# Optimization experiments

Measured on AMD Instinct MI355X. Metric: run time of the kernel, lower is better.

The kernel has to match this reference:

```python
import jax, jax.numpy as jnp
import numpy as np

D_MODEL = 1024
NUM_HEADS = 16
D_K = D_MODEL // NUM_HEADS


def setup_inputs() -> dict:
    key = jax.random.key(0)
    ks = jax.random.split(key, 16)
    B, S, D = 4, 2048, D_MODEL
    scale = 1.0 / np.sqrt(D)
    inp = {
        'Xs': jax.random.normal(ks[0], (B, S, D), jnp.float32),
        'Xt': jax.random.normal(ks[1], (B, S, D), jnp.float32),
    }
    names = ['qs', 'qt', 'ks', 'kt', 'vs', 'vt']
    for i, n in enumerate(names):
        inp['W_' + n] = jax.random.normal(ks[2 + 2 * i], (D, D), jnp.float32) * scale
        inp['b_' + n] = jax.random.normal(ks[3 + 2 * i], (D,), jnp.float32) * 0.01
    inp['attn_bias'] = jnp.zeros((1, 1, 1, 1), jnp.float32)
    return inp


def _split_heads(x):
    B, S, _ = x.shape
    return x.reshape(B, S, NUM_HEADS, D_K).transpose(0, 2, 1, 3)  # (B,H,S,dk)


def reference(Xs, Xt, W_qs, b_qs, W_qt, b_qt, W_ks, b_ks, W_kt, b_kt,
              W_vs, b_vs, W_vt, b_vt, attn_bias):
    # Dual-linear fused projections: Linear(x) = x @ W.T + b (torch convention)
    Q = Xs @ W_qs.T + b_qs + Xt @ W_qt.T + b_qt
    K = Xs @ W_ks.T + b_ks + Xt @ W_kt.T + b_kt
    V = Xs @ W_vs.T + b_vs + Xt @ W_vt.T + b_vt
    Q, K, V = _split_heads(Q), _split_heads(K), _split_heads(V)
    scores = jnp.einsum('bhqd,bhkd->bhqk', Q, K) / jnp.sqrt(jnp.float32(D_K))
    scores = scores + attn_bias  # scalar learned bias, broadcast
    probs = jax.nn.softmax(scores, axis=-1)
    out = jnp.einsum('bhqk,bhkd->bhqd', probs, V)  # (B,H,S,dk)
    B, H, S, dk = out.shape
    return out.transpose(0, 2, 1, 3).reshape(B, S, H * dk)
```

## Files before the change

kernel.cpp:

```cpp
#include <hip/hip_runtime.h>
#include <hip/hip_bf16.h>

typedef __bf16 bf16;
typedef __attribute__((ext_vector_type(8))) __bf16 bf16x8;
typedef __attribute__((ext_vector_type(4))) __bf16 bf16x4;
typedef __attribute__((ext_vector_type(4))) float f32x4;

#define D_MODEL 1024
#define NHEAD 16
#define DK 64
#define BB 4
#define SS 2048
#define MM 8192
#define KK 2048
#define NN 3072

#define LDP 72
#define QSCALE 0.18033688011112042f

__device__ __forceinline__ void glds16(const bf16* g, bf16* s) {
    __builtin_amdgcn_global_load_lds(
        (const __attribute__((address_space(1))) void*)g,
        (__attribute__((address_space(3))) void*)s, 16, 0, 0);
}

__global__ void cast_pack(const float* __restrict__ src, bf16* __restrict__ dst,
                          int row_off, int col_off, int nchunks) {
    int i = blockIdx.x * 256 + threadIdx.x;
    if (i >= nchunks) return;
    int m = i >> 7;
    int cl = i & 127;
    const float4* s4 = (const float4*)&src[((size_t)m << 10) + cl * 8];
    float4 v0 = s4[0], v1 = s4[1];
    bf16x8 o;
    o[0]=(bf16)v0.x; o[1]=(bf16)v0.y; o[2]=(bf16)v0.z; o[3]=(bf16)v0.w;
    o[4]=(bf16)v1.x; o[5]=(bf16)v1.y; o[6]=(bf16)v1.z; o[7]=(bf16)v1.w;
    int r = row_off + m;
    int k = col_off + cl * 8;
    int mi = r & 127, mt = r >> 7;
    int c = (k >> 3) & 7, kt = k >> 6;
    int slot = mi * 8 + (c ^ (mi & 7));
    *(bf16x8*)&dst[(((((size_t)mt * 32 + kt) << 10) + slot) << 3)] = o;
}

__global__ void bias_cat_k(const float* __restrict__ bqs, const float* __restrict__ bqt,
                           const float* __restrict__ bks, const float* __restrict__ bkt,
                           const float* __restrict__ bvs, const float* __restrict__ bvt,
                           float* __restrict__ out) {
    int n = blockIdx.x * 256 + threadIdx.x;
    int g = n >> 10, c = n & 1023;
    const float* a = (g == 0) ? bqs : ((g == 1) ? bks : bvs);
    const float* b = (g == 0) ? bqt : ((g == 1) ? bkt : bvt);
    out[n] = a[c] + b[c];
}

__global__ __launch_bounds__(256) void gemm_qkv(
    const bf16* __restrict__ Xp, const bf16* __restrict__ Wp,
    const float* __restrict__ biasc,
    bf16* __restrict__ Qb, bf16* __restrict__ Kb, bf16* __restrict__ Vt) {
    __shared__ __align__(16) bf16 sA[128 * 64];
    __shared__ __align__(16) bf16 sB[128 * 64];

    const int m0 = blockIdx.x * 128, n0 = blockIdx.y * 128;
    const int t = threadIdx.x, lane = t & 63, w = t >> 6;
    const int quad = lane >> 4, l16 = lane & 15, swz = l16 & 7;
    const int wm = (w >> 1) * 64, wn = (w & 1) * 64;

    f32x4 acc[4][4] = {};

    for (int ktI = 0; ktI < 32; ktI++) {
        const bf16* Ab = Xp + (((size_t)blockIdx.x * 32 + ktI) << 13);
        const bf16* Bb = Wp + (((size_t)blockIdx.y * 32 + ktI) << 13);
#pragma unroll
        for (int j = 0; j < 4; j++) {
            int u = (w * 4 + j) * 64 + lane;
            glds16(Ab + (size_t)u * 8, &sA[(w * 4 + j) * 512]);
            glds16(Bb + (size_t)u * 8, &sB[(w * 4 + j) * 512]);
        }
        __syncthreads();
#pragma unroll
        for (int kb = 0; kb < 2; kb++) {
            bf16x8 af[4], bfr[4];
#pragma unroll
            for (int mi = 0; mi < 4; mi++)
                af[mi] = *(const bf16x8*)&sA[(wm + mi * 16 + l16) * 64 + (((kb * 4 + quad) ^ swz) * 8)];
#pragma unroll
            for (int ni = 0; ni < 4; ni++)
                bfr[ni] = *(const bf16x8*)&sB[(wn + ni * 16 + l16) * 64 + (((kb * 4 + quad) ^ swz) * 8)];
#pragma unroll
            for (int mi = 0; mi < 4; mi++)
#pragma unroll
                for (int ni = 0; ni < 4; ni++)
                    acc[mi][ni] = __builtin_amdgcn_mfma_f32_16x16x32_bf16(
                        af[mi], bfr[ni], acc[mi][ni], 0, 0, 0);
        }
        __syncthreads();
    }

    const int g = n0 >> 10;
    for (int mi = 0; mi < 4; mi++) {
        int mbase = m0 + wm + mi * 16 + quad * 4;
        for (int ni = 0; ni < 4; ni++) {
            int n = n0 + wn + ni * 16 + l16;
            float bias = biasc[n];
            int c = n & 1023, h = c >> 6, d = c & 63;
            for (int r = 0; r < 4; r++) {
                int m = mbase + r;
                int b = m >> 11, s = m & 2047;
                size_t bh = (size_t)(b * NHEAD + h);
                float v = acc[mi][ni][r] + bias;
                if (g == 0)
                    Qb[(bh * SS + s) * DK + d] = (bf16)(v * QSCALE);
                else if (g == 1)
                    Kb[(bh * SS + s) * DK + d] = (bf16)v;
                else
                    Vt[(bh * DK + d) * SS + s] = (bf16)v;
            }
        }
    }
}

__global__ __launch_bounds__(256) void attn(
    const bf16* __restrict__ Qb, const bf16* __restrict__ Kb,
    const bf16* __restrict__ Vt, float* __restrict__ out) {
    __shared__ __align__(16) bf16 sK[64 * 64];
    __shared__ __align__(16) bf16 sV[64 * 64];
    __shared__ __align__(16) bf16 sP[4][32 * LDP];

    const int q0 = blockIdx.x * 128;
    const int bh = blockIdx.y;
    const int t = threadIdx.x;
    const int lane = t & 63, w = t >> 6;
    const int quad = lane >> 4, l16 = lane & 15, swz = l16 & 7;
    const int b = bh >> 4, h = bh & 15;

    const bf16* Qp = Qb + ((size_t)bh * SS + q0 + w * 32) * DK;
    bf16x8 qf[2][2];
#pragma unroll
    for (int f = 0; f < 2; f++)
#pragma unroll
        for (int kb = 0; kb < 2; kb++)
            qf[f][kb] = *(const bf16x8*)&Qp[(f * 16 + l16) * DK + kb * 32 + quad * 8];

    f32x4 o[2][4] = {};
    float lsum[2] = {0.f, 0.f};

    const bf16* Kp = Kb + (size_t)bh * SS * DK;
    const bf16* Vp = Vt + (size_t)bh * DK * SS;

    for (int kt = 0; kt < SS; kt += 64) {
#pragma unroll
        for (int j = 0; j < 2; j++) {
            int u = (w * 2 + j) * 64 + lane;
            int row = u >> 3;
            int cc = (u & 7) ^ (row & 7);
            glds16(Kp + (size_t)(kt + row) * DK + cc * 8, &sK[(w * 2 + j) * 512]);
            glds16(Vp + (size_t)row * SS + kt + cc * 8, &sV[(w * 2 + j) * 512]);
        }
        __syncthreads();

        f32x4 st[2][4] = {};
#pragma unroll
        for (int kb = 0; kb < 2; kb++)
#pragma unroll
            for (int ki = 0; ki < 4; ki++) {
                bf16x8 kf = *(const bf16x8*)&sK[(ki * 16 + l16) * 64 + (((kb * 4 + quad) ^ swz) * 8)];
                st[0][ki] = __builtin_amdgcn_mfma_f32_16x16x32_bf16(kf, qf[0][kb], st[0][ki], 0, 0, 0);
                st[1][ki] = __builtin_amdgcn_mfma_f32_16x16x32_bf16(kf, qf[1][kb], st[1][ki], 0, 0, 0);
            }

#pragma unroll
        for (int f = 0; f < 2; f++) {
            float ls = 0.f;
#pragma unroll
            for (int ki = 0; ki < 4; ki++) {
                float p0 = __builtin_amdgcn_exp2f(st[f][ki][0]);
                float p1 = __builtin_amdgcn_exp2f(st[f][ki][1]);
                float p2 = __builtin_amdgcn_exp2f(st[f][ki][2]);
                float p3 = __builtin_amdgcn_exp2f(st[f][ki][3]);
                ls += (p0 + p1) + (p2 + p3);
                bf16x4 pk;
                pk[0] = (bf16)p0; pk[1] = (bf16)p1; pk[2] = (bf16)p2; pk[3] = (bf16)p3;
                *(bf16x4*)&sP[w][(f * 16 + l16) * LDP + ki * 16 + quad * 4] = pk;
            }
            lsum[f] += ls;
        }

#pragma unroll
        for (int kb = 0; kb < 2; kb++) {
            bf16x8 af0 = *(const bf16x8*)&sP[w][(l16) * LDP + kb * 32 + quad * 8];
            bf16x8 af1 = *(const bf16x8*)&sP[w][(16 + l16) * LDP + kb * 32 + quad * 8];
#pragma unroll
            for (int ni = 0; ni < 4; ni++) {
                bf16x8 vf = *(const bf16x8*)&sV[(ni * 16 + l16) * 64 + (((kb * 4 + quad) ^ swz) * 8)];
                o[0][ni] = __builtin_amdgcn_mfma_f32_16x16x32_bf16(af0, vf, o[0][ni], 0, 0, 0);
                o[1][ni] = __builtin_amdgcn_mfma_f32_16x16x32_bf16(af1, vf, o[1][ni], 0, 0, 0);
            }
        }
        __syncthreads();
    }

#pragma unroll
    for (int f = 0; f < 2; f++) {
        lsum[f] += __shfl_xor(lsum[f], 16);
        lsum[f] += __shfl_xor(lsum[f], 32);
    }

    float* op = out + ((size_t)(b * SS + q0 + w * 32)) * D_MODEL + h * DK;
#pragma unroll
    for (int f = 0; f < 2; f++)
#pragma unroll
        for (int r = 0; r < 4; r++) {
            float linv = 1.0f / __shfl(lsum[f], quad * 4 + r);
#pragma unroll
            for (int ni = 0; ni < 4; ni++)
                op[(f * 16 + quad * 4 + r) * D_MODEL + ni * 16 + l16] = o[f][ni][r] * linv;
        }
}

extern "C" void kernel_launch(void* const* d_in, const int* in_sizes, int n_in,
                              void* d_out, int out_size, void* d_ws, size_t ws_size,
                              hipStream_t stream) {
    const float* Xs   = (const float*)d_in[0];
    const float* Xt   = (const float*)d_in[1];
    const float* Wqs  = (const float*)d_in[2];
    const float* bqs  = (const float*)d_in[3];
    const float* Wqt  = (const float*)d_in[4];
    const float* bqt  = (const float*)d_in[5];
    const float* Wks  = (const float*)d_in[6];
    const float* bks  = (const float*)d_in[7];
    const float* Wkt  = (const float*)d_in[8];
    const float* bkt  = (const float*)d_in[9];
    const float* Wvs  = (const float*)d_in[10];
    const float* bvs  = (const float*)d_in[11];
    const float* Wvt  = (const float*)d_in[12];
    const float* bvt  = (const float*)d_in[13];
    float* out = (float*)d_out;

    char* ws = (char*)d_ws;
    bf16*  Xp    = (bf16*)(ws);
    bf16*  Wp    = (bf16*)(ws + 33554432);
    float* biasc = (float*)(ws + 46137344);
    bf16*  Qb    = (bf16*)(ws + 46149632);
    bf16*  Kb    = (bf16*)(ws + 62926848);
    bf16*  Vt    = (bf16*)(ws + 79704064);

    {
        int nchunks = MM * 128;
        int blocks = nchunks / 256;
        cast_pack<<<blocks, 256, 0, stream>>>(Xs, Xp, 0, 0, nchunks);
        cast_pack<<<blocks, 256, 0, stream>>>(Xt, Xp, 0, 1024, nchunks);
    }
    {
        int nchunks = 1024 * 128;
        int blocks = nchunks / 256;
        const float* Wsrc_s[3] = {Wqs, Wks, Wvs};
        const float* Wsrc_t[3] = {Wqt, Wkt, Wvt};
        for (int gi = 0; gi < 3; gi++) {
            cast_pack<<<blocks, 256, 0, stream>>>(Wsrc_s[gi], Wp, gi * 1024, 0, nchunks);
            cast_pack<<<blocks, 256, 0, stream>>>(Wsrc_t[gi], Wp, gi * 1024, 1024, nchunks);
        }
    }
    bias_cat_k<<<12, 256, 0, stream>>>(bqs, bqt, bks, bkt, bvs, bvt, biasc);

    gemm_qkv<<<dim3(MM / 128, NN / 128), 256, 0, stream>>>(Xp, Wp, biasc, Qb, Kb, Vt);

    attn<<<dim3(SS / 128, BB * NHEAD), 256, 0, stream>>>(Qb, Kb, Vt, out);
}
```

Baseline: 381.1 us.

## Double attention query tile per block and merge cast/bias kernels

The attention kernel now gives each block 256 queries, 64 rows per wave, instead of 128. K and V fragments are loaded from shared memory once into registers and reused across four query row-groups, which halves the total K/V global loads and LDS reads per query. The eight cast_pack launches plus the bias kernel are merged into two launches to cut launch overhead. In exchange the attention grid shrinks to 512 blocks and register and LDS use per block rise, which may lower occupancy and latency hiding.

Result: slower. 400.9 us (+5.2%).

```diff
diff --git a/kernel.cpp b/kernel.cpp
--- a/kernel.cpp
+++ b/kernel.cpp
@@ -24,12 +24,11 @@
         (__attribute__((address_space(3))) void*)s, 16, 0, 0);
 }
 
-__global__ void cast_pack(const float* __restrict__ src, bf16* __restrict__ dst,
-                          int row_off, int col_off, int nchunks) {
-    int i = blockIdx.x * 256 + threadIdx.x;
-    if (i >= nchunks) return;
-    int m = i >> 7;
-    int cl = i & 127;
+__device__ __forceinline__ void pack_chunk(const float* __restrict__ src,
+                                           bf16* __restrict__ dst,
+                                           int row_off, int col_off, int idx) {
+    int m = idx >> 7;
+    int cl = idx & 127;
     const float4* s4 = (const float4*)&src[((size_t)m << 10) + cl * 8];
     float4 v0 = s4[0], v1 = s4[1];
     bf16x8 o;
@@ -43,15 +42,36 @@
     *(bf16x8*)&dst[(((((size_t)mt * 32 + kt) << 10) + slot) << 3)] = o;
 }
 
-__global__ void bias_cat_k(const float* __restrict__ bqs, const float* __restrict__ bqt,
-                           const float* __restrict__ bks, const float* __restrict__ bkt,
-                           const float* __restrict__ bvs, const float* __restrict__ bvt,
-                           float* __restrict__ out) {
-    int n = blockIdx.x * 256 + threadIdx.x;
-    int g = n >> 10, c = n & 1023;
-    const float* a = (g == 0) ? bqs : ((g == 1) ? bks : bvs);
-    const float* b = (g == 0) ? bqt : ((g == 1) ? bkt : bvt);
-    out[n] = a[c] + b[c];
+__global__ void pack_x(const float* __restrict__ Xs, const float* __restrict__ Xt,
+                       bf16* __restrict__ dst) {
+    int i = blockIdx.x * 256 + threadIdx.x;
+    int sel = i >> 20;
+    int idx = i & 1048575;
+    pack_chunk(sel ? Xt : Xs, dst, 0, sel ? 1024 : 0, idx);
+}
+
+__global__ void pack_w(const float* __restrict__ Wqs, const float* __restrict__ Wqt,
+                       const float* __restrict__ Wks, const float* __restrict__ Wkt,
+                       const float* __restrict__ Wvs, const float* __restrict__ Wvt,
+                       const float* __restrict__ bqs, const float* __restrict__ bqt,
+                       const float* __restrict__ bks, const float* __restrict__ bkt,
+                       const float* __restrict__ bvs, const float* __restrict__ bvt,
+                       bf16* __restrict__ dst, float* __restrict__ biasc) {
+    if (blockIdx.x == 3072) {
+        for (int n = threadIdx.x; n < NN; n += 256) {
+            int g = n >> 10, c = n & 1023;
+            const float* a = (g == 0) ? bqs : ((g == 1) ? bks : bvs);
+            const float* b = (g == 0) ? bqt : ((g == 1) ? bkt : bvt);
+            biasc[n] = a[c] + b[c];
+        }
+        return;
+    }
+    int i = blockIdx.x * 256 + threadIdx.x;
+    int gi = i >> 17;
+    int idx = i & 131071;
+    const float* src = (gi == 0) ? Wqs : (gi == 1) ? Wqt : (gi == 2) ? Wks
+                     : (gi == 3) ? Wkt : (gi == 4) ? Wvs : Wvt;
+    pack_chunk(src, dst, (gi >> 1) * 1024, (gi & 1) * 1024, idx);
 }
 
 __global__ __launch_bounds__(256) void gemm_qkv(
@@ -125,25 +145,25 @@
     const bf16* __restrict__ Vt, float* __restrict__ out) {
     __shared__ __align__(16) bf16 sK[64 * 64];
     __shared__ __align__(16) bf16 sV[64 * 64];
-    __shared__ __align__(16) bf16 sP[4][32 * LDP];
-
-    const int q0 = blockIdx.x * 128;
+    __shared__ __align__(16) bf16 sP[4][64 * LDP];
+
+    const int q0 = blockIdx.x * 256;
     const int bh = blockIdx.y;
     const int t = threadIdx.x;
     const int lane = t & 63, w = t >> 6;
     const int quad = lane >> 4, l16 = lane & 15, swz = l16 & 7;
     const int b = bh >> 4, h = bh & 15;
 
-    const bf16* Qp = Qb + ((size_t)bh * SS + q0 + w * 32) * DK;
-    bf16x8 qf[2][2];
-#pragma unroll
-    for (int f = 0; f < 2; f++)
+    const bf16* Qp = Qb + ((size_t)bh * SS + q0 + w * 64) * DK;
+    bf16x8 qf[4][2];
+#pragma unroll
+    for (int f = 0; f < 4; f++)
 #pragma unroll
         for (int kb = 0; kb < 2; kb++)
             qf[f][kb] = *(const bf16x8*)&Qp[(f * 16 + l16) * DK + kb * 32 + quad * 8];
 
-    f32x4 o[2][4] = {};
-    float lsum[2] = {0.f, 0.f};
+    f32x4 o[4][4] = {};
+    float lsum[4] = {0.f, 0.f, 0.f, 0.f};
 
     const bf16* Kp = Kb + (size_t)bh * SS * DK;
     const bf16* Vp = Vt + (size_t)bh * DK * SS;
@@ -159,25 +179,30 @@
         }
         __syncthreads();
 
-        f32x4 st[2][4] = {};
+        bf16x8 kf[2][4];
 #pragma unroll
         for (int kb = 0; kb < 2; kb++)
 #pragma unroll
+            for (int ki = 0; ki < 4; ki++)
+                kf[kb][ki] = *(const bf16x8*)&sK[(ki * 16 + l16) * 64 + (((kb * 4 + quad) ^ swz) * 8)];
+
+#pragma unroll
+        for (int f = 0; f < 4; f++) {
+            f32x4 st[4] = {};
+#pragma unroll
+            for (int kb = 0; kb < 2; kb++)
+#pragma unroll
+                for (int ki = 0; ki < 4; ki++)
+                    st[ki] = __builtin_amdgcn_mfma_f32_16x16x32_bf16(
+                        kf[kb][ki], qf[f][kb], st[ki], 0, 0, 0);
+
+            float ls = 0.f;
+#pragma unroll
             for (int ki = 0; ki < 4; ki++) {
-                bf16x8 kf = *(const bf16x8*)&sK[(ki * 16 + l16) * 64 + (((kb * 4 + quad) ^ swz) * 8)];
-                st[0][ki] = __builtin_amdgcn_mfma_f32_16x16x32_bf16(kf, qf[0][kb], st[0][ki], 0, 0, 0);
-                st[1][ki] = __builtin_amdgcn_mfma_f32_16x16x32_bf16(kf, qf[1][kb], st[1][ki], 0, 0, 0);
-            }
-
-#pragma unroll
-        for (int f = 0; f < 2; f++) {
-            float ls = 0.f;
-#pragma unroll
-            for (int ki = 0; ki < 4; ki++) {
-                float p0 = __builtin_amdgcn_exp2f(st[f][ki][0]);
-                float p1 = __builtin_amdgcn_exp2f(st[f][ki][1]);
-                float p2 = __builtin_amdgcn_exp2f(st[f][ki][2]);
-                float p3 = __builtin_amdgcn_exp2f(st[f][ki][3]);
+                float p0 = __builtin_amdgcn_exp2f(st[ki][0]);
+                float p1 = __builtin_amdgcn_exp2f(st[ki][1]);
+                float p2 = __builtin_amdgcn_exp2f(st[ki][2]);
+                float p3 = __builtin_amdgcn_exp2f(st[ki][3]);
                 ls += (p0 + p1) + (p2 + p3);
                 bf16x4 pk;
                 pk[0] = (bf16)p0; pk[1] = (bf16)p1; pk[2] = (bf16)p2; pk[3] = (bf16)p3;
@@ -186,29 +211,35 @@
             lsum[f] += ls;
         }
 
-#pragma unroll
-        for (int kb = 0; kb < 2; kb++) {
-            bf16x8 af0 = *(const bf16x8*)&sP[w][(l16) * LDP + kb * 32 + quad * 8];
-            bf16x8 af1 = *(const bf16x8*)&sP[w][(16 + l16) * LDP + kb * 32 + quad * 8];
-#pragma unroll
-            for (int ni = 0; ni < 4; ni++) {
-                bf16x8 vf = *(const bf16x8*)&sV[(ni * 16 + l16) * 64 + (((kb * 4 + quad) ^ swz) * 8)];
-                o[0][ni] = __builtin_amdgcn_mfma_f32_16x16x32_bf16(af0, vf, o[0][ni], 0, 0, 0);
-                o[1][ni] = __builtin_amdgcn_mfma_f32_16x16x32_bf16(af1, vf, o[1][ni], 0, 0, 0);
+        bf16x8 vf[2][4];
+#pragma unroll
+        for (int kb = 0; kb < 2; kb++)
+#pragma unroll
+            for (int ni = 0; ni < 4; ni++)
+                vf[kb][ni] = *(const bf16x8*)&sV[(ni * 16 + l16) * 64 + (((kb * 4 + quad) ^ swz) * 8)];
+
+#pragma unroll
+        for (int f = 0; f < 4; f++)
+#pragma unroll
+            for (int kb = 0; kb < 2; kb++) {
+                bf16x8 af = *(const bf16x8*)&sP[w][(f * 16 + l16) * LDP + kb * 32 + quad * 8];
+#pragma unroll
+                for (int ni = 0; ni < 4; ni++)
+                    o[f][ni] = __builtin_amdgcn_mfma_f32_16x16x32_bf16(
+                        af, vf[kb][ni], o[f][ni], 0, 0, 0);
             }
-        }
-        __syncthreads();
-    }
-
-#pragma unroll
-    for (int f = 0; f < 2; f++) {
+        __syncthreads();
+    }
+
+#pragma unroll
+    for (int f = 0; f < 4; f++) {
         lsum[f] += __shfl_xor(lsum[f], 16);
         lsum[f] += __shfl_xor(lsum[f], 32);
     }
 
-    float* op = out + ((size_t)(b * SS + q0 + w * 32)) * D_MODEL + h * DK;
-#pragma unroll
-    for (int f = 0; f < 2; f++)
+    float* op = out + ((size_t)(b * SS + q0 + w * 64)) * D_MODEL + h * DK;
+#pragma unroll
+    for (int f = 0; f < 4; f++)
 #pragma unroll
         for (int r = 0; r < 4; r++) {
             float linv = 1.0f / __shfl(lsum[f], quad * 4 + r);
@@ -245,25 +276,11 @@
     bf16*  Kb    = (bf16*)(ws + 62926848);
     bf16*  Vt    = (bf16*)(ws + 79704064);
 
-    {
-        int nchunks = MM * 128;
-        int blocks = nchunks / 256;
-        cast_pack<<<blocks, 256, 0, stream>>>(Xs, Xp, 0, 0, nchunks);
-        cast_pack<<<blocks, 256, 0, stream>>>(Xt, Xp, 0, 1024, nchunks);
-    }
-    {
-        int nchunks = 1024 * 128;
-        int blocks = nchunks / 256;
-        const float* Wsrc_s[3] = {Wqs, Wks, Wvs};
-        const float* Wsrc_t[3] = {Wqt, Wkt, Wvt};
-        for (int gi = 0; gi < 3; gi++) {
-            cast_pack<<<blocks, 256, 0, stream>>>(Wsrc_s[gi], Wp, gi * 1024, 0, nchunks);
-            cast_pack<<<blocks, 256, 0, stream>>>(Wsrc_t[gi], Wp, gi * 1024, 1024, nchunks);
-        }
-    }
-    bias_cat_k<<<12, 256, 0, stream>>>(bqs, bqt, bks, bkt, bvs, bvt, biasc);
+    pack_x<<<8192, 256, 0, stream>>>(Xs, Xt, Xp);
+    pack_w<<<3073, 256, 0, stream>>>(Wqs, Wqt, Wks, Wkt, Wvs, Wvt,
+                                     bqs, bqt, bks, bkt, bvs, bvt, Wp, biasc);
 
     gemm_qkv<<<dim3(MM / 128, NN / 128), 256, 0, stream>>>(Xp, Wp, biasc, Qb, Kb, Vt);
 
-    attn<<<dim3(SS / 128, BB * NHEAD), 256, 0, stream>>>(Qb, Kb, Vt, out);
-}
+    attn<<<dim3(SS / 256, BB * NHEAD), 256, 0, stream>>>(Qb, Kb, Vt, out);
+}
```
